# Kernel optimization log

Measured on AMD Instinct MI355X. Metric: run time of the kernel, lower is better.

## Reference

```python
import jax, jax.numpy as jnp
import numpy as np
from jax import lax

V_PATCH_NUMS = (1, 2, 3, 4, 5, 6, 8, 10, 13, 16)
SHARE_K = 4
RESI = 0.5  # abs(quant_resi)


def _area_matrix(pn, H):
    # F.interpolate(mode='area') == adaptive_avg_pool2d: uniform mean over [floor, ceil) window
    W = np.zeros((pn, H), np.float32)
    for i in range(pn):
        s = int(np.floor(i * H / pn)); e = int(np.ceil((i + 1) * H / pn))
        W[i, s:e] = 1.0 / (e - s)
    return W


def _cubic(x, a=-0.75):
    x = abs(x)
    if x <= 1.0:
        return (a + 2) * x**3 - (a + 3) * x**2 + 1
    if x < 2.0:
        return a * x**3 - 5 * a * x**2 + 8 * a * x - 4 * a
    return 0.0


def _bicubic_matrix(out, inp):
    # torch bicubic, align_corners=False, a=-0.75, border-clamped (separable 1D matrix)
    W = np.zeros((out, inp), np.float32)
    for i in range(out):
        src = (i + 0.5) * inp / out - 0.5
        i0 = int(np.floor(src)); t = src - i0
        for k in range(-1, 3):
            j = min(max(i0 + k, 0), inp - 1)
            W[i, j] += _cubic(k - t)
    return W


def _phi_select(si, SN, K=SHARE_K):
    ticks = np.linspace(1 / 3 / K, 1 - 1 / 3 / K, K) if K == 4 else np.linspace(1 / 2 / K, 1 - 1 / 2 / K, K)
    return int(np.argmin(np.abs(ticks - si / (SN - 1))))


def _phi(h, w, b):
    # Phi: h*(1-r) + conv3x3(h)*r
    y = lax.conv_general_dilated(h, w, (1, 1), 'SAME',
                                 dimension_numbers=('NCHW', 'OIHW', 'NCHW'))
    y = y + b[None, :, None, None]
    return h * (1.0 - RESI) + y * RESI


def reference(f, embedding, phi_w, phi_b):
    # Multi-scale residual vector quantization (VectorQuantizer2 hot path).
    # f: [B, C, 16, 16] latent; embedding: [V, C]; phi_w: [K, C, C, 3, 3]; phi_b: [K, C]
    B, C, H, Wd = f.shape
    SN = len(V_PATCH_NUMS)
    e2 = jnp.sum(embedding**2, axis=1)  # [V]
    f_hat = jnp.zeros_like(f)
    f_rest = f
    for si, pn in enumerate(V_PATCH_NUMS):
        if si != SN - 1:
            A = jnp.asarray(_area_matrix(pn, H))
            z = jnp.einsum('ph,bchw,qw->bcpq', A, f_rest, A)  # area downsample to pn x pn
        else:
            z = f_rest
        zf = z.transpose(0, 2, 3, 1).reshape(-1, C)  # [B*pn*pn, C]
        # squared-distance cdist + argmin codebook lookup
        d = jnp.sum(zf**2, axis=1, keepdims=True) - 2.0 * (zf @ embedding.T) + e2[None, :]
        idx = jnp.argmin(d, axis=1)  # [B*pn*pn]
        h = embedding[idx].reshape(B, pn, pn, C).transpose(0, 3, 1, 2)  # gather -> [B,C,pn,pn]
        if si != SN - 1:
            U = jnp.asarray(_bicubic_matrix(H, pn))
            h = jnp.einsum('hp,bcpq,wq->bchw', U, h, U)  # bicubic upsample to H x W
        k = _phi_select(si, SN)
        h = _phi(h, phi_w[k], phi_b[k])  # partially-shared Phi residual refinement
        f_hat = f_hat + h
        f_rest = f_rest - h
    return f_hat


def setup_inputs() -> dict:
    key = jax.random.key(0)
    k1, k2, k3 = jax.random.split(key, 3)
    f = jax.random.normal(k1, (64, 32, 16, 16), dtype=jnp.float32)
    embedding = jax.random.normal(k2, (4096, 32), dtype=jnp.float32)
    phi_w = jax.random.normal(k3, (4, 32, 32, 3, 3), dtype=jnp.float32) * 0.05
    phi_b = jnp.zeros((4, 32), dtype=jnp.float32)
    return {"f": f, "embedding": embedding, "phi_w": phi_w, "phi_b": phi_b}
```

## Files before the change

kernel.cpp:

```cpp
#include <hip/hip_runtime.h>
#include <cmath>


#define BB 64
#define CC 32
#define HH 16
#define VV 4096
#define NTOT (BB*CC*HH*HH)

typedef __attribute__((ext_vector_type(8))) short bf16x8;
typedef __attribute__((ext_vector_type(4))) float f32x4;

__device__ __forceinline__ double cubicw(double x) {
    x = fabs(x);
    const double a = -0.75;
    if (x <= 1.0) return ((a + 2.0) * x - (a + 3.0)) * x * x + 1.0;
    if (x < 2.0)  return (((a * x - 5.0 * a) * x + 8.0 * a) * x - 4.0 * a);
    return 0.0;
}

__device__ __forceinline__ unsigned int ordf(float d) {
    unsigned int b = __float_as_uint(d);
    return (b & 0x80000000u) ? ~b : (b | 0x80000000u);
}

__device__ __forceinline__ short f2bf(float x) {
    unsigned u = __float_as_uint(x);
    unsigned r = (u + 0x7fffu + ((u >> 16) & 1u)) >> 16;
    return (short)r;
}
__device__ __forceinline__ float bf2f(short h) {
    return __uint_as_float(((unsigned)(unsigned short)h) << 16);
}

__global__ void init_k(const float* __restrict__ f, const float* __restrict__ E,
                       float* __restrict__ f_rest, float* __restrict__ f_hat,
                       float* __restrict__ e2, float* __restrict__ z,
                       float* __restrict__ es) {
    int i = blockIdx.x * 256 + threadIdx.x;
    if (i < NTOT) { f_rest[i] = f[i]; f_hat[i] = 0.f; }
    if (i < VV) {
        float s = 0.f;
        unsigned short* ew = es ? (unsigned short*)(es + (size_t)i * 48) : (unsigned short*)0;
        #pragma unroll
        for (int c = 0; c < CC; ++c) {
            float x = E[i * CC + c];
            s += x * x;
            if (ew) {
                short h = f2bf(x); float rm = x - bf2f(h);
                short m = f2bf(rm); float rl = rm - bf2f(m);
                short l = f2bf(rl);
                ew[c] = (unsigned short)h;
                ew[32 + c] = (unsigned short)m;
                ew[64 + c] = (unsigned short)l;
            }
        }
        e2[i] = s;
    }
    if (i < BB * CC) {
        const float* src = f + (size_t)i * (HH * HH);
        float s = 0.f;
        for (int j = 0; j < HH * HH; ++j) s += src[j];
        z[i] = s * (1.0f / 256.0f);
    }
}

__global__ __launch_bounds__(256, 4) void argsmall_k(const float* __restrict__ z,
        const float* __restrict__ E, const float* __restrict__ e2,
        unsigned long long* __restrict__ bestk, int M, int G, int gsz) {
    const int t = threadIdx.x;
    int m = blockIdx.x * 64 + (t & 63);
    int w = __builtin_amdgcn_readfirstlane(t >> 6);
    int wg = blockIdx.y * 4 + w;
    int v0 = wg * gsz;
    float zr[CC]; float z2 = 0.f;
    const float4* zp = (const float4*)(z + (size_t)m * CC);
    #pragma unroll
    for (int c4 = 0; c4 < 8; ++c4) {
        float4 v = zp[c4];
        zr[c4*4+0] = v.x; zr[c4*4+1] = v.y; zr[c4*4+2] = v.z; zr[c4*4+3] = v.w;
        z2 += v.x*v.x + v.y*v.y + v.z*v.z + v.w*v.w;
    }
    const float* e = E + (size_t)v0 * CC;
    float best = 3.4e38f; int bv = v0;
    for (int v = v0; v < v0 + gsz; v += 2, e += 2 * CC) {
        float a0 = 0.f, a1 = 0.f, b0 = 0.f, b1 = 0.f;
        #pragma unroll
        for (int c = 0; c < CC; c += 2) {
            a0 = fmaf(zr[c],   e[c],      a0);
            a1 = fmaf(zr[c+1], e[c+1],    a1);
            b0 = fmaf(zr[c],   e[CC+c],   b0);
            b1 = fmaf(zr[c+1], e[CC+c+1], b1);
        }
        float dA = fmaf(-2.f, a0 + a1, z2 + e2[v]);
        float dB = fmaf(-2.f, b0 + b1, z2 + e2[v+1]);
        if (dA < best) { best = dA; bv = v; }
        if (dB < best) { best = dB; bv = v + 1; }
    }
    bestk[(size_t)m * G + wg] = ((unsigned long long)ordf(best) << 32) |
                                (unsigned long long)(unsigned int)bv;
}

__global__ __launch_bounds__(256, 4) void argmf_k(const unsigned short* __restrict__ zs,
        const float* __restrict__ es, const float* __restrict__ e2,
        unsigned long long* __restrict__ bestk, int M, int G, int gsz) {
    __shared__ float s_es[128 * 52];
    __shared__ float s_e2[128];
    const int t = threadIdx.x;
    const int g = blockIdx.y;
    const int v0 = g * gsz;
    for (int i = t; i < gsz * 12; i += 256) {
        int row = i / 12, part = i - row * 12;
        *(float4*)&s_es[row * 52 + part * 4] =
            *(const float4*)&es[(size_t)(v0 + row) * 48 + part * 4];
    }
    for (int i = t; i < gsz; i += 256) s_e2[i] = e2[v0 + i];

    const int lane = t & 63;
    const int w = t >> 6;
    const int n = lane & 15, kq = lane >> 4;

    int tb[2]; bf16x8 ah[2], am[2], al[2];
    #pragma unroll
    for (int pt = 0; pt < 2; ++pt) {
        int tb0 = blockIdx.x * 128 + w * 32 + pt * 16;
        if (tb0 > M - 16) tb0 = M - 16;
        tb[pt] = tb0;
        const unsigned short* zp = zs + (size_t)(tb0 + n) * 96 + kq * 8;
        ah[pt] = *(const bf16x8*)(zp);
        am[pt] = *(const bf16x8*)(zp + 32);
        al[pt] = *(const bf16x8*)(zp + 64);
    }
    __syncthreads();

    float bd[2][4]; int bc[2][4];
    #pragma unroll
    for (int pt = 0; pt < 2; ++pt)
        #pragma unroll
        for (int r = 0; r < 4; ++r) { bd[pt][r] = 3.4e38f; bc[pt][r] = 0; }

    const int nct = gsz >> 4;
    for (int ct = 0; ct < nct; ++ct) {
        int base = (ct * 16 + n) * 52 + kq * 4;
        bf16x8 eh = *(const bf16x8*)&s_es[base];
        bf16x8 em = *(const bf16x8*)&s_es[base + 16];
        bf16x8 el = *(const bf16x8*)&s_es[base + 32];
        float e2c = s_e2[ct * 16 + n];
        #pragma unroll
        for (int pt = 0; pt < 2; ++pt) {
            f32x4 Ca = {0.f, 0.f, 0.f, 0.f};
            f32x4 Cb = {0.f, 0.f, 0.f, 0.f};
            Ca = __builtin_amdgcn_mfma_f32_16x16x32_bf16(ah[pt], eh, Ca, 0, 0, 0);
            Cb = __builtin_amdgcn_mfma_f32_16x16x32_bf16(am[pt], eh, Cb, 0, 0, 0);
            Ca = __builtin_amdgcn_mfma_f32_16x16x32_bf16(ah[pt], em, Ca, 0, 0, 0);
            Cb = __builtin_amdgcn_mfma_f32_16x16x32_bf16(al[pt], eh, Cb, 0, 0, 0);
            Ca = __builtin_amdgcn_mfma_f32_16x16x32_bf16(ah[pt], el, Ca, 0, 0, 0);
            Cb = __builtin_amdgcn_mfma_f32_16x16x32_bf16(am[pt], em, Cb, 0, 0, 0);
            #pragma unroll
            for (int r = 0; r < 4; ++r) {
                float d = fmaf(-2.f, Cb[r], e2c);
                d = fmaf(-2.f, Ca[r], d);
                if (d < bd[pt][r]) { bd[pt][r] = d; bc[pt][r] = ct; }
            }
        }
    }
    #pragma unroll
    for (int pt = 0; pt < 2; ++pt) {
        #pragma unroll
        for (int r = 0; r < 4; ++r) {
            int v = v0 + bc[pt][r] * 16 + n;
            unsigned long long k = ((unsigned long long)ordf(bd[pt][r]) << 32) |
                                   (unsigned long long)(unsigned int)v;
            #pragma unroll
            for (int msk = 1; msk < 16; msk <<= 1) {
                unsigned long long o = __shfl_xor(k, msk);
                if (o < k) k = o;
            }
            if (n == 0)
                bestk[(size_t)(tb[pt] + kq * 4 + r) * G + g] = k;
        }
    }
}

__global__ __launch_bounds__(256, 4) void argbig_k(const float* __restrict__ z,
        const float* __restrict__ E, const float* __restrict__ e2,
        unsigned long long* __restrict__ bestk, int M, int G, int gsz) {
    __shared__ float s_e[128 * CC];
    __shared__ float s_e2[128];
    const int T = gridDim.x * 256;
    const int g = blockIdx.y;
    const int v0 = g * gsz;
    {
        const float4* src = (const float4*)(E + (size_t)v0 * CC);
        float4* dst = (float4*)s_e;
        for (int i = threadIdx.x; i < gsz * 8; i += 256) dst[i] = src[i];
        if (threadIdx.x < gsz) s_e2[threadIdx.x] = e2[v0 + threadIdx.x];
    }
    int   mm[2];
    bool  act[2];
    float zr[2][CC];
    float z2[2];
    #pragma unroll
    for (int pt = 0; pt < 2; ++pt) {
        int m0 = blockIdx.x * 256 + threadIdx.x + pt * T;
        act[pt] = (m0 < M);
        int m = act[pt] ? m0 : M - 1;
        mm[pt] = m;
        const float4* zp = (const float4*)(z + (size_t)m * CC);
        float zz = 0.f;
        #pragma unroll
        for (int c4 = 0; c4 < 8; ++c4) {
            float4 v = zp[c4];
            zr[pt][c4*4+0] = v.x; zr[pt][c4*4+1] = v.y;
            zr[pt][c4*4+2] = v.z; zr[pt][c4*4+3] = v.w;
            zz += v.x*v.x + v.y*v.y + v.z*v.z + v.w*v.w;
        }
        z2[pt] = zz;
    }
    __syncthreads();
    float best[2]; int bv[2];
    #pragma unroll
    for (int pt = 0; pt < 2; ++pt) { best[pt] = 3.4e38f; bv[pt] = v0; }
    const float4* ev = (const float4*)s_e;
    for (int vi = 0; vi < gsz; ++vi, ev += 8) {
        float4 e0 = ev[0], e1 = ev[1], e2v = ev[2], e3 = ev[3];
        float4 e4 = ev[4], e5 = ev[5], e6v = ev[6], e7 = ev[7];
        float ef[CC] = {e0.x,e0.y,e0.z,e0.w, e1.x,e1.y,e1.z,e1.w,
                        e2v.x,e2v.y,e2v.z,e2v.w, e3.x,e3.y,e3.z,e3.w,
                        e4.x,e4.y,e4.z,e4.w, e5.x,e5.y,e5.z,e5.w,
                        e6v.x,e6v.y,e6v.z,e6v.w, e7.x,e7.y,e7.z,e7.w};
        float a0 = 0.f, a1 = 0.f, b0 = 0.f, b1 = 0.f;
        #pragma unroll
        for (int c = 0; c < CC; c += 2) {
            a0 = fmaf(zr[0][c],   ef[c],   a0);
            a1 = fmaf(zr[0][c+1], ef[c+1], a1);
            b0 = fmaf(zr[1][c],   ef[c],   b0);
            b1 = fmaf(zr[1][c+1], ef[c+1], b1);
        }
        float e2c = s_e2[vi];
        float dA = fmaf(-2.f, a0 + a1, z2[0] + e2c);
        float dB = fmaf(-2.f, b0 + b1, z2[1] + e2c);
        int v = v0 + vi;
        if (dA < best[0]) { best[0] = dA; bv[0] = v; }
        if (dB < best[1]) { best[1] = dB; bv[1] = v; }
    }
    #pragma unroll
    for (int pt = 0; pt < 2; ++pt)
        if (act[pt])
            bestk[(size_t)mm[pt] * G + g] =
                ((unsigned long long)ordf(best[pt]) << 32) |
                (unsigned long long)(unsigned int)bv[pt];
}

__global__ __launch_bounds__(512) void fuse_k(const unsigned long long* __restrict__ bestk,
                      const float* __restrict__ E,
                      const float* __restrict__ pw, const float* __restrict__ pb,
                      float* __restrict__ f_hat, float* __restrict__ f_rest,
                      float* __restrict__ z_next, unsigned short* __restrict__ zsn,
                      int pn, int G, int TPP, int kphi, int pnn) {
    __shared__ float s_buf[CC * 18 * 20];
    __shared__ float s_pw[CC * 9 * 8];
    __shared__ float s_part[256 * 9];
    __shared__ int   s_idx[256];
    __shared__ float s_w[HH][4];
    __shared__ int   s_j[HH][4];
    __shared__ unsigned long long s_red[512];
    const int t   = threadIdx.x;
    const int cog = blockIdx.x;
    const int b   = blockIdx.y;
    const int P   = pn * pn;
    const int half = t >> 8;
    const int tl   = t & 255;

    {
        int p = t / TPP, sub = t - p * TPP;
        unsigned long long bk = ~0ull;
        if (p < P) {
            const unsigned long long* kp = bestk + (size_t)(b * P + p) * G;
            for (int gg = sub; gg < G; gg += TPP) {
                unsigned long long o = kp[gg];
                if (o < bk) bk = o;
            }
        }
        s_red[t] = bk;
        __syncthreads();
        for (int s = TPP >> 1; s > 0; s >>= 1) {
            if ((sub < s) && p < P) {
                unsigned long long o = s_red[t + s];
                if (o < s_red[t]) s_red[t] = o;
            }
            __syncthreads();
        }
        if (t < P) s_idx[t] = (int)(unsigned int)(s_red[t * TPP] & 0xffffffffull);
    }
    if (t < HH) {
        double src = (t + 0.5) * (double)pn / 16.0 - 0.5;
        double fi = floor(src); int i0 = (int)fi; double tt = src - fi;
        #pragma unroll
        for (int k = 0; k < 4; ++k) {
            int j = i0 - 1 + k; j = j < 0 ? 0 : (j > pn - 1 ? pn - 1 : j);
            s_j[t][k] = j;
            s_w[t][k] = (float)cubicw((double)(k - 1) - tt);
        }
    }
    {
        const float* src = pw + ((size_t)(kphi * CC + cog * 8)) * CC * 9;
        for (int i = t; i < 8 * CC * 9; i += 512) {
            int col = i / (CC * 9);
            int r   = i - col * (CC * 9);
            s_pw[r * 8 + col] = src[i];
        }
    }
    __syncthreads();

    if (tl < HH * pn) {
        int h = tl / pn, q = tl % pn;
        int cbase = half * 16;
        float acc[16];
        #pragma unroll
        for (int c = 0; c < 16; ++c) acc[c] = 0.f;
        #pragma unroll
        for (int k = 0; k < 4; ++k) {
            float wv = s_w[h][k];
            if (wv == 0.0f) continue;
            int row = s_idx[s_j[h][k] * pn + q];
            const float4* er = (const float4*)(E + (size_t)row * CC + cbase);
            #pragma unroll
            for (int c4 = 0; c4 < 4; ++c4) {
                float4 e4 = er[c4];
                acc[c4*4+0] = fmaf(wv, e4.x, acc[c4*4+0]);
                acc[c4*4+1] = fmaf(wv, e4.y, acc[c4*4+1]);
                acc[c4*4+2] = fmaf(wv, e4.z, acc[c4*4+2]);
                acc[c4*4+3] = fmaf(wv, e4.w, acc[c4*4+3]);
            }
        }
        #pragma unroll
        for (int c = 0; c < 16; ++c)
            s_buf[((cbase + c) * HH + h) * pn + q] = acc[c];
    }
    __syncthreads();

    {
        int h = tl >> 4, w = tl & 15;
        int cbase = half * 16;
        float acc[16];
        #pragma unroll
        for (int c = 0; c < 16; ++c) acc[c] = 0.f;
        #pragma unroll
        for (int k = 0; k < 4; ++k) {
            float wh = s_w[w][k];
            int j = s_j[w][k];
            #pragma unroll
            for (int c = 0; c < 16; ++c)
                acc[c] = fmaf(wh, s_buf[((cbase + c) * HH + h) * pn + j], acc[c]);
        }
        __syncthreads();
        #pragma unroll
        for (int c = 0; c < 16; ++c)
            s_buf[((cbase + c) * 18 + h + 1) * 20 + w + 1] = acc[c];
        if (w == 0) {
            #pragma unroll
            for (int c = 0; c < 16; ++c) s_buf[((cbase + c) * 18 + h + 1) * 20] = 0.f;
        }
        if (w >= 13) {
            #pragma unroll
            for (int c = 0; c < 16; ++c) s_buf[((cbase + c) * 18 + h + 1) * 20 + w + 4] = 0.f;
        }
        if (h == 0) {
            #pragma unroll
            for (int c = 0; c < 16; ++c) {
                s_buf[((cbase + c) * 18) * 20 + w] = 0.f;
                if (w < 4) s_buf[((cbase + c) * 18) * 20 + 16 + w] = 0.f;
            }
        }
        if (h == 15) {
            #pragma unroll
            for (int c = 0; c < 16; ++c) {
                s_buf[((cbase + c) * 18 + 17) * 20 + w] = 0.f;
                if (w < 4) s_buf[((cbase + c) * 18 + 17) * 20 + 16 + w] = 0.f;
            }
        }
    }
    __syncthreads();

    int col = tl >> 5;
    int co  = cog * 8 + col;
    int s   = tl & 31;
    int h   = s >> 1;
    int w0  = (s & 1) * 8;
    float acc[8];
    float bias = pb[kphi * CC + co];
    #pragma unroll
    for (int o = 0; o < 8; ++o) acc[o] = (half == 0) ? bias : 0.f;
    int ci0 = half * 16;
    for (int ci = ci0; ci < ci0 + 16; ++ci) {
        const float* wb = &s_pw[(ci * 9) * 8 + col];
        #pragma unroll
        for (int kh = 0; kh < 3; ++kh) {
            const float4* xr = (const float4*)&s_buf[(ci * 18 + h + kh) * 20 + w0];
            float4 a0 = xr[0], a1 = xr[1], a2 = xr[2];
            float xf[12] = {a0.x, a0.y, a0.z, a0.w, a1.x, a1.y, a1.z, a1.w,
                            a2.x, a2.y, a2.z, a2.w};
            float k0 = wb[(kh*3+0)*8], k1 = wb[(kh*3+1)*8], k2 = wb[(kh*3+2)*8];
            #pragma unroll
            for (int o = 0; o < 8; ++o)
                acc[o] += xf[o] * k0 + xf[o+1] * k1 + xf[o+2] * k2;
        }
    }
    if (half == 1) {
        #pragma unroll
        for (int o = 0; o < 8; ++o) s_part[tl * 9 + o] = acc[o];
    }
    __syncthreads();

    float4 r0, r1;
    if (half == 0) {
        #pragma unroll
        for (int o = 0; o < 8; ++o) acc[o] += s_part[tl * 9 + o];
        size_t base = ((size_t)(b * CC + co) * HH + h) * HH + w0;
        float hf[8];
        #pragma unroll
        for (int o = 0; o < 8; ++o) {
            float hv = s_buf[(co * 18 + h + 1) * 20 + w0 + o + 1];
            hf[o] = 0.5f * hv + 0.5f * acc[o];
        }
        float4* fh = (float4*)(f_hat + base);
        float4* fr = (float4*)(f_rest + base);
        float4 v0 = fh[0], v1 = fh[1];
        v0.x += hf[0]; v0.y += hf[1]; v0.z += hf[2]; v0.w += hf[3];
        v1.x += hf[4]; v1.y += hf[5]; v1.z += hf[6]; v1.w += hf[7];
        fh[0] = v0; fh[1] = v1;
        r0 = fr[0]; r1 = fr[1];
        r0.x -= hf[0]; r0.y -= hf[1]; r0.z -= hf[2]; r0.w -= hf[3];
        r1.x -= hf[4]; r1.y -= hf[5]; r1.z -= hf[6]; r1.w -= hf[7];
        fr[0] = r0; fr[1] = r1;
    }

    if (pnn > 0) {
        __syncthreads();
        float* fn = s_buf;
        if (half == 0) {
            float* d = &fn[(col * HH + h) * HH + w0];
            d[0] = r0.x; d[1] = r0.y; d[2] = r0.z; d[3] = r0.w;
            d[4] = r1.x; d[5] = r1.y; d[6] = r1.z; d[7] = r1.w;
        }
        __syncthreads();
        int P2 = pnn * pnn;
        for (int i = t; i < P2 * 8; i += 512) {
            int cl = i & 7, pq = i >> 3;
            int q2 = pq % pnn, p2 = pq / pnn;
            int sp = (p2 * HH) / pnn, ep = ((p2 + 1) * HH + pnn - 1) / pnn;
            int sq = (q2 * HH) / pnn, eq = ((q2 + 1) * HH + pnn - 1) / pnn;
            float wgt = 1.0f / ((float)(ep - sp) * (float)(eq - sq));
            float sum = 0.f;
            for (int h2 = sp; h2 < ep; ++h2)
                for (int w2 = sq; w2 < eq; ++w2)
                    sum += fn[(cl * HH + h2) * HH + w2];
            float v = sum * wgt;
            int c = cog * 8 + cl;
            if (zsn) {
                size_t baz = (size_t)(b * P2 + pq) * 96 + c;
                unsigned short hh = (unsigned short)f2bf(v);
                float rm = v - bf2f((short)hh);
                unsigned short mm2 = (unsigned short)f2bf(rm);
                float rl = rm - bf2f((short)mm2);
                unsigned short ll = (unsigned short)f2bf(rl);
                zsn[baz] = hh; zsn[baz + 32] = mm2; zsn[baz + 64] = ll;
            } else {
                z_next[((size_t)(b * P2 + pq)) * CC + c] = v;
            }
        }
    }
}

extern "C" void kernel_launch(void* const* d_in, const int* in_sizes, int n_in,
                              void* d_out, int out_size, void* d_ws, size_t ws_size,
                              hipStream_t stream) {
    const float* f  = (const float*)d_in[0];
    const float* E  = (const float*)d_in[1];
    const float* pw = (const float*)d_in[2];
    const float* pb = (const float*)d_in[3];
    float* out = (float*)d_out;

    const size_t need_base = (size_t)(NTOT + VV) * 4 + (size_t)524288 * 8 +
                             (size_t)524288 * 4;
    const size_t need_mf = need_base + (size_t)VV * 48 * 4 +
                           (size_t)16384 * 96 * 2;
    const bool use_mf = (ws_size >= need_mf);

    float* wsf    = (float*)d_ws;
    float* f_rest = wsf;
    float* e2     = wsf + (size_t)NTOT;
    unsigned long long* bestk = (unsigned long long*)(e2 + VV);
    float* z      = (float*)(bestk + 524288);
    float* es     = use_mf ? (z + 524288) : (float*)0;
    unsigned short* zs = use_mf ? (unsigned short*)(es + (size_t)VV * 48) : (unsigned short*)0;

    int phik[10];
    {
        double start = 1.0 / 3.0 / 4.0;
        double stop  = 1.0 - 1.0 / 3.0 / 4.0;
        double step  = (stop - start) / 3.0;
        double ticks[4];
        for (int i = 0; i < 4; ++i) ticks[i] = (double)i * step + start;
        ticks[3] = stop;
        for (int si = 0; si < 10; ++si) {
            double s = (double)si / 9.0;
            int bk = 0; double bd = fabs(ticks[0] - s);
            for (int tq = 1; tq < 4; ++tq) {
                double d2 = fabs(ticks[tq] - s);
                if (d2 < bd) { bd = d2; bk = tq; }
            }
            phik[si] = bk;
        }
    }

    static const int pns[10]  = {1, 2, 3, 4, 5, 6, 8, 10, 13, 16};
    static const int grpS[10] = {256, 128, 64, 32, 32, 16, 0, 0, 0, 0};
    static const int grpF[10] = {0, 0, 0, 0, 0, 0, 128, 64, 32, 32};
    static const int grpM[10] = {0, 0, 0, 0, 0, 0, 32, 32, 32, 32};

    init_k<<<(NTOT + 255) / 256, 256, 0, stream>>>(f, E, f_rest, out, e2, z, es);

    for (int si = 0; si < 10; ++si) {
        int pn = pns[si];
        int P = pn * pn;
        int M = BB * P;
        int G, TPP;
        if (pn <= 6) {
            int grp = grpS[si];
            G = grp * 4;
            int gsz = VV / G;
            argsmall_k<<<dim3(P, grp), 256, 0, stream>>>(z, E, e2, bestk, M, G, gsz);
        } else if (use_mf) {
            G = grpM[si];
            int gsz = VV / G;
            int bx = (M + 127) / 128;
            argmf_k<<<dim3(bx, G), 256, 0, stream>>>(zs, es, e2, bestk, M, G, gsz);
        } else {
            G = grpF[si];
            int gsz = VV / G;
            int bx = (M + 511) / 512;
            argbig_k<<<dim3(bx, G), 256, 0, stream>>>(z, E, e2, bestk, M, G, gsz);
        }
        TPP = 1;
        while (TPP * 2 * P <= 512) TPP *= 2;
        int pnn = (si < 9) ? pns[si + 1] : 0;
        unsigned short* zsn = (pnn >= 8 && use_mf) ? zs : (unsigned short*)0;
        fuse_k<<<dim3(4, BB), 512, 0, stream>>>(bestk, E, pw, pb,
                                                out, f_rest, z, zsn,
                                                pn, G, TPP, phik[si], pnn);
    }
}
```

Baseline: 452.8 us.

## Fold -2 scale and e2 into MFMA accumulators; restructure Phi conv register blocking

```diff
diff --git a/kernel.cpp b/kernel.cpp
--- a/kernel.cpp
+++ b/kernel.cpp
@@ -149,7 +149,7 @@
         #pragma unroll
         for (int pt = 0; pt < 2; ++pt) {
             f32x4 Ca = {0.f, 0.f, 0.f, 0.f};
-            f32x4 Cb = {0.f, 0.f, 0.f, 0.f};
+            f32x4 Cb = {e2c, e2c, e2c, e2c};
             Ca = __builtin_amdgcn_mfma_f32_16x16x32_bf16(ah[pt], eh, Ca, 0, 0, 0);
             Cb = __builtin_amdgcn_mfma_f32_16x16x32_bf16(am[pt], eh, Cb, 0, 0, 0);
             Ca = __builtin_amdgcn_mfma_f32_16x16x32_bf16(ah[pt], em, Ca, 0, 0, 0);
@@ -158,8 +158,7 @@
             Cb = __builtin_amdgcn_mfma_f32_16x16x32_bf16(am[pt], em, Cb, 0, 0, 0);
             #pragma unroll
             for (int r = 0; r < 4; ++r) {
-                float d = fmaf(-2.f, Cb[r], e2c);
-                d = fmaf(-2.f, Ca[r], d);
+                float d = Ca[r] + Cb[r];
                 if (d < bd[pt][r]) { bd[pt][r] = d; bc[pt][r] = ct; }
             }
         }
@@ -259,8 +258,8 @@
                       float* __restrict__ z_next, unsigned short* __restrict__ zsn,
                       int pn, int G, int TPP, int kphi, int pnn) {
     __shared__ float s_buf[CC * 18 * 20];
-    __shared__ float s_pw[CC * 9 * 8];
-    __shared__ float s_part[256 * 9];
+    __shared__ float s_pw[CC * 3 * 4 * 8];
+    __shared__ float s_part[3 * 128 * 20];
     __shared__ int   s_idx[256];
     __shared__ float s_w[HH][4];
     __shared__ int   s_j[HH][4];
@@ -306,9 +305,12 @@
     {
         const float* src = pw + ((size_t)(kphi * CC + cog * 8)) * CC * 9;
         for (int i = t; i < 8 * CC * 9; i += 512) {
-            int col = i / (CC * 9);
-            int r   = i - col * (CC * 9);
-            s_pw[r * 8 + col] = src[i];
+            int l  = i / (CC * 9);
+            int r  = i - l * (CC * 9);
+            int ci = r / 9; int kk = r - ci * 9;
+            int kh = kk / 3; int kw = kk - kh * 3;
+            int cp = l >> 1, ce = l & 1;
+            s_pw[ci * 96 + kh * 32 + cp * 8 + ce * 4 + kw] = src[i];
         }
     }
     __syncthreads();
@@ -383,66 +385,98 @@
     }
     __syncthreads();
 
-    int col = tl >> 5;
-    int co  = cog * 8 + col;
-    int s   = tl & 31;
-    int h   = s >> 1;
-    int w0  = (s & 1) * 8;
-    float acc[8];
-    float bias = pb[kphi * CC + co];
-    #pragma unroll
-    for (int o = 0; o < 8; ++o) acc[o] = (half == 0) ? bias : 0.f;
-    int ci0 = half * 16;
-    for (int ci = ci0; ci < ci0 + 16; ++ci) {
-        const float* wb = &s_pw[(ci * 9) * 8 + col];
-        #pragma unroll
-        for (int kh = 0; kh < 3; ++kh) {
+    const int cp  = tl >> 6;
+    const int q   = (tl >> 5) & 1;
+    const int s   = tl & 31;
+    const int h   = s >> 1;
+    const int w0  = (s & 1) * 8;
+    const int wid = half * 2 + q;
+    const int pos = cp * 32 + s;
+    float accE[8], accO[8];
+    #pragma unroll
+    for (int o = 0; o < 8; ++o) { accE[o] = 0.f; accO[o] = 0.f; }
+    const int ci0 = wid * 8;
+    for (int ci = ci0; ci < ci0 + 8; ++ci) {
+        const float* wrow = &s_pw[ci * 96 + cp * 8];
+        #pragma unroll
+        for (int kk = 0; kk < 3; ++kk) {
+            int kh = kk + q; kh = (kh >= 3) ? kh - 3 : kh;
             const float4* xr = (const float4*)&s_buf[(ci * 18 + h + kh) * 20 + w0];
             float4 a0 = xr[0], a1 = xr[1], a2 = xr[2];
             float xf[12] = {a0.x, a0.y, a0.z, a0.w, a1.x, a1.y, a1.z, a1.w,
                             a2.x, a2.y, a2.z, a2.w};
-            float k0 = wb[(kh*3+0)*8], k1 = wb[(kh*3+1)*8], k2 = wb[(kh*3+2)*8];
-            #pragma unroll
-            for (int o = 0; o < 8; ++o)
-                acc[o] += xf[o] * k0 + xf[o+1] * k1 + xf[o+2] * k2;
-        }
-    }
-    if (half == 1) {
-        #pragma unroll
-        for (int o = 0; o < 8; ++o) s_part[tl * 9 + o] = acc[o];
+            const float4* wp = (const float4*)(wrow + kh * 32);
+            float4 wA = wp[0];
+            float4 wB = wp[1];
+            #pragma unroll
+            for (int o = 0; o < 8; ++o) {
+                accE[o] += xf[o] * wA.x + xf[o+1] * wA.y + xf[o+2] * wA.z;
+                accO[o] += xf[o] * wB.x + xf[o+1] * wB.y + xf[o+2] * wB.z;
+            }
+        }
+    }
+    if (wid != 0) {
+        float* dst = &s_part[((wid - 1) * 128 + pos) * 20];
+        *(float4*)(dst +  0) = make_float4(accE[0], accE[1], accE[2], accE[3]);
+        *(float4*)(dst +  4) = make_float4(accE[4], accE[5], accE[6], accE[7]);
+        *(float4*)(dst +  8) = make_float4(accO[0], accO[1], accO[2], accO[3]);
+        *(float4*)(dst + 12) = make_float4(accO[4], accO[5], accO[6], accO[7]);
     }
     __syncthreads();
 
-    float4 r0, r1;
-    if (half == 0) {
-        #pragma unroll
-        for (int o = 0; o < 8; ++o) acc[o] += s_part[tl * 9 + o];
-        size_t base = ((size_t)(b * CC + co) * HH + h) * HH + w0;
-        float hf[8];
-        #pragma unroll
-        for (int o = 0; o < 8; ++o) {
-            float hv = s_buf[(co * 18 + h + 1) * 20 + w0 + o + 1];
-            hf[o] = 0.5f * hv + 0.5f * acc[o];
-        }
-        float4* fh = (float4*)(f_hat + base);
-        float4* fr = (float4*)(f_rest + base);
-        float4 v0 = fh[0], v1 = fh[1];
-        v0.x += hf[0]; v0.y += hf[1]; v0.z += hf[2]; v0.w += hf[3];
-        v1.x += hf[4]; v1.y += hf[5]; v1.z += hf[6]; v1.w += hf[7];
-        fh[0] = v0; fh[1] = v1;
-        r0 = fr[0]; r1 = fr[1];
-        r0.x -= hf[0]; r0.y -= hf[1]; r0.z -= hf[2]; r0.w -= hf[3];
-        r1.x -= hf[4]; r1.y -= hf[5]; r1.z -= hf[6]; r1.w -= hf[7];
-        fr[0] = r0; fr[1] = r1;
+    float4 rE0, rE1, rO0, rO1;
+    if (wid == 0) {
+        #pragma unroll
+        for (int g2 = 0; g2 < 3; ++g2) {
+            const float* sp = &s_part[(g2 * 128 + pos) * 20];
+            float4 p0 = *(const float4*)(sp + 0), p1 = *(const float4*)(sp + 4);
+            float4 p2 = *(const float4*)(sp + 8), p3 = *(const float4*)(sp + 12);
+            accE[0] += p0.x; accE[1] += p0.y; accE[2] += p0.z; accE[3] += p0.w;
+            accE[4] += p1.x; accE[5] += p1.y; accE[6] += p1.z; accE[7] += p1.w;
+            accO[0] += p2.x; accO[1] += p2.y; accO[2] += p2.z; accO[3] += p2.w;
+            accO[4] += p3.x; accO[5] += p3.y; accO[6] += p3.z; accO[7] += p3.w;
+        }
+        float biasE = pb[kphi * CC + cog * 8 + cp * 2];
+        float biasO = pb[kphi * CC + cog * 8 + cp * 2 + 1];
+        #pragma unroll
+        for (int o = 0; o < 8; ++o) { accE[o] += biasE; accO[o] += biasO; }
+        #pragma unroll
+        for (int c = 0; c < 2; ++c) {
+            const float* acc = c ? accO : accE;
+            int co = cog * 8 + cp * 2 + c;
+            float hf[8];
+            #pragma unroll
+            for (int o = 0; o < 8; ++o) {
+                float hv = s_buf[(co * 18 + h + 1) * 20 + w0 + o + 1];
+                hf[o] = 0.5f * hv + 0.5f * acc[o];
+            }
+            size_t base = ((size_t)(b * CC + co) * HH + h) * HH + w0;
+            float4* fh = (float4*)(f_hat + base);
+            float4* fr = (float4*)(f_rest + base);
+            float4 v0 = fh[0], v1 = fh[1];
+            v0.x += hf[0]; v0.y += hf[1]; v0.z += hf[2]; v0.w += hf[3];
+            v1.x += hf[4]; v1.y += hf[5]; v1.z += hf[6]; v1.w += hf[7];
+            fh[0] = v0; fh[1] = v1;
+            float4 r0 = fr[0], r1 = fr[1];
+            r0.x -= hf[0]; r0.y -= hf[1]; r0.z -= hf[2]; r0.w -= hf[3];
+            r1.x -= hf[4]; r1.y -= hf[5]; r1.z -= hf[6]; r1.w -= hf[7];
+            fr[0] = r0; fr[1] = r1;
+            if (c) { rO0 = r0; rO1 = r1; } else { rE0 = r0; rE1 = r1; }
+        }
     }
 
     if (pnn > 0) {
         __syncthreads();
         float* fn = s_buf;
-        if (half == 0) {
-            float* d = &fn[(col * HH + h) * HH + w0];
-            d[0] = r0.x; d[1] = r0.y; d[2] = r0.z; d[3] = r0.w;
-            d[4] = r1.x; d[5] = r1.y; d[6] = r1.z; d[7] = r1.w;
+        if (wid == 0) {
+            #pragma unroll
+            for (int c = 0; c < 2; ++c) {
+                int cl = cp * 2 + c;
+                float* d = &fn[(cl * HH + h) * HH + w0];
+                float4 r0 = c ? rO0 : rE0, r1 = c ? rO1 : rE1;
+                d[0] = r0.x; d[1] = r0.y; d[2] = r0.z; d[3] = r0.w;
+                d[4] = r1.x; d[5] = r1.y; d[6] = r1.z; d[7] = r1.w;
+            }
         }
         __syncthreads();
         int P2 = pnn * pnn;
@@ -459,9 +493,10 @@
             float v = sum * wgt;
             int c = cog * 8 + cl;
             if (zsn) {
+                float tv = -2.0f * v;
                 size_t baz = (size_t)(b * P2 + pq) * 96 + c;
-                unsigned short hh = (unsigned short)f2bf(v);
-                float rm = v - bf2f((short)hh);
+                unsigned short hh = (unsigned short)f2bf(tv);
+                float rm = tv - bf2f((short)hh);
                 unsigned short mm2 = (unsigned short)f2bf(rm);
                 float rl = rm - bf2f((short)mm2);
                 unsigned short ll = (unsigned short)f2bf(rl);
```

After: 416.2 us. 1.09x faster.
